# Performance work log

Measured on AMD Instinct MI355X. Metric: run time of the kernel, lower is better.

## Reference

```python
import jax, jax.numpy as jnp
import numpy as np

K = 3       # kernel_size
RATE = 2    # dilation rate
NH = 8      # num_heads
EPS = 1e-5  # InstanceNorm eps


def _conv1x1(x, W, b):
    # x: [B,C,H,W], W: [O,C], b: [O]
    return jnp.einsum('bchw,oc->bohw', x, W) + b[None, :, None, None]


def _inorm(x):
    mu = jnp.mean(x, axis=(2, 3), keepdims=True)
    var = jnp.var(x, axis=(2, 3), keepdims=True)
    return (x - mu) / jnp.sqrt(var + EPS)


def _extract_patches(x):
    # dilated KxK patches, stride 1, 'same' grid -> [B, C, K*K, H, W]
    B, C, H, W = x.shape
    pad = RATE * (K - 1) // 2
    xp = jnp.pad(x, ((0, 0), (0, 0), (pad, pad), (pad, pad)))
    taps = [xp[:, :, i * RATE:i * RATE + H, j * RATE:j * RATE + W]
            for i in range(K) for j in range(K)]
    return jnp.stack(taps, axis=2)


def setup_inputs() -> dict:
    key = jax.random.key(0)
    ks = jax.random.split(key, 8)
    B, C, H, W, A = 1, 64, 64, 64, 128
    features = jax.random.normal(ks[0], (B, C, H, W), jnp.float32)
    masks = jax.random.uniform(ks[1], (B, 1, H, W), jnp.float32)
    s_in = 1.0 / np.sqrt(C).astype(np.float32)
    Wq = jax.random.normal(ks[2], (A, C), jnp.float32) * s_in
    bq = jnp.zeros((A,), jnp.float32)
    Wk = jax.random.normal(ks[3], (A, C), jnp.float32) * s_in
    bk = jnp.zeros((A,), jnp.float32)
    Wo = jax.random.normal(ks[4], (C, C), jnp.float32) * s_in
    bo = jnp.zeros((C,), jnp.float32)
    return dict(features=features, masks=masks, Wq=Wq, bq=bq,
                Wk=Wk, bk=bk, Wo=Wo, bo=bo)


def reference(features, masks, Wq, bq, Wk, bk, Wo, bo):
    B, C, H, W = features.shape
    A = Wq.shape[0]
    hc = A // NH
    L = H * W
    KK = K * K

    m = (masks > 0.5).astype(features.dtype)          # 1 = hole
    f_masked = features * m
    f_unmasked = features * (1.0 - m)

    q = jax.nn.relu(_inorm(_conv1x1(f_masked, Wq, bq)))    # [B,A,H,W]
    k = jax.nn.relu(_inorm(_conv1x1(f_unmasked, Wk, bk)))  # [B,A,H,W]

    # per-head dilated patch banks: [B,NH,hc*KK,L]
    qp = _extract_patches(q).reshape(B, NH, hc * KK, L)
    kp = _extract_patches(k).reshape(B, NH, hc * KK, L)

    # patch-correlation attention per head: [B,NH,L,L]
    attn = jax.nn.softmax(jnp.einsum('bndq,bndk->bnqk', qp, kp), axis=-1)

    # value patch bank from unmasked features: [B,C*KK,L]
    vp = _extract_patches(f_unmasked).reshape(B, C * KK, L)

    # sample value patches: [B,NH,L,C*KK]
    sampled = jnp.einsum('bnqk,bdk->bnqd', attn, vp)

    # fold: average the KK taps per channel, then average over heads
    attended = sampled.reshape(B, NH, L, C, KK).mean(axis=4).mean(axis=1)  # [B,L,C]
    attended = attended.transpose(0, 2, 1).reshape(B, C, H, W)

    return jax.nn.relu(_inorm(_conv1x1(attended, Wo, bo)))
```

## Files before the change

### kernel.cpp

```cpp
#include <hip/hip_runtime.h>
#include <hip/hip_bf16.h>


#define LL 4096
#define CC 64
#define AA 128
#define NH_ 8
#define KSTR 168
#define VSTR 72
#define LOG2E 1.44269504088896340736f

typedef _Float16 half8 __attribute__((ext_vector_type(8)));
typedef float floatx4 __attribute__((ext_vector_type(4)));

__device__ __forceinline__ float fexp2(float x) {
    float r;
    asm("v_exp_f32 %0, %1" : "=v"(r) : "v"(x));
    return r;
}

__global__ __launch_bounds__(256) void prep_kernel(
    const float* __restrict__ feat,
    const float* __restrict__ masks,
    const float* __restrict__ Wq, const float* __restrict__ bq,
    const float* __restrict__ Wk, const float* __restrict__ bk,
    _Float16* __restrict__ q_act, _Float16* __restrict__ k_act,
    _Float16* __restrict__ vb)
{
    const int tid = threadIdx.x;
    const int b = blockIdx.x;
    __shared__ float sW[CC];
    __shared__ float sm[8];

    if (b >= 2 * AA) {
        int c = b - 2 * AA;
        for (int p = 0; p < 16; ++p) {
            int l = p * 256 + tid;
            int y = l >> 6, x = l & 63;
            float s = 0.f;
            for (int ty = 0; ty < 3; ++ty) {
                int yy = y + 2 * (ty - 1);
                if (yy < 0 || yy > 63) continue;
                for (int tx = 0; tx < 3; ++tx) {
                    int xx = x + 2 * (tx - 1);
                    if (xx < 0 || xx > 63) continue;
                    int ll = yy * 64 + xx;
                    float hole = masks[ll] > 0.5f ? 1.f : 0.f;
                    s += feat[c * LL + ll] * (1.f - hole);
                }
            }
            vb[c * LL + l] = (_Float16)(s * (1.f / 9.f));
        }
        return;
    }

    const int a = b & (AA - 1);
    const int sel = b >> 7;
    const float* Wrow = (sel ? Wk : Wq) + a * CC;
    const float bias = sel ? bk[a] : bq[a];
    if (tid < CC) sW[tid] = Wrow[tid];
    __syncthreads();

    float acc[16];
#pragma unroll
    for (int p = 0; p < 16; ++p) acc[p] = 0.f;
    for (int c = 0; c < CC; ++c) {
        float wc = sW[c];
        const float* fr = feat + (size_t)c * LL + tid;
#pragma unroll
        for (int p = 0; p < 16; ++p) acc[p] += wc * fr[p * 256];
    }

    float vals[16];
    float s1 = 0.f, s2 = 0.f;
#pragma unroll
    for (int p = 0; p < 16; ++p) {
        int l = p * 256 + tid;
        float hole = masks[l] > 0.5f ? 1.f : 0.f;
        float mf = sel ? (1.f - hole) : hole;
        float v = acc[p] * mf + bias;
        vals[p] = v; s1 += v; s2 += v * v;
    }
    for (int off = 32; off; off >>= 1) {
        s1 += __shfl_down(s1, off, 64);
        s2 += __shfl_down(s2, off, 64);
    }
    int wv = tid >> 6, ln = tid & 63;
    if (ln == 0) { sm[wv * 2] = s1; sm[wv * 2 + 1] = s2; }
    __syncthreads();
    s1 = sm[0] + sm[2] + sm[4] + sm[6];
    s2 = sm[1] + sm[3] + sm[5] + sm[7];
    float mu = s1 * (1.f / LL);
    float inv = rsqrtf(s2 * (1.f / LL) - mu * mu + 1e-5f);

    const float oscale = sel ? 1.f : LOG2E;
    _Float16* act = (sel ? k_act : q_act) + (size_t)a * LL;
#pragma unroll
    for (int p = 0; p < 16; ++p) {
        int l = p * 256 + tid;
        float v = (vals[p] - mu) * inv;
        act[l] = (_Float16)(v > 0.f ? v * oscale : 0.f);
    }
}

__global__ __launch_bounds__(256) void build_kp(
    const _Float16* __restrict__ k_act, _Float16* __restrict__ kp)
{
    const int n = blockIdx.x, y = blockIdx.y;
    const int tid = threadIdx.x;
    const _Float16* ka = k_act + (size_t)n * 16 * LL;
    _Float16* base = kp + ((size_t)n * LL + y * 64) * KSTR;
#pragma unroll
    for (int i = 0; i < 6; ++i) {
        int idx = tid + i * 256;
        if (idx >= 64 * 21) break;
        int x = idx / 21, c21 = idx - x * 21;
        half8 v8;
#pragma unroll
        for (int j = 0; j < 8; ++j) {
            int d = c21 * 8 + j;
            _Float16 v = (_Float16)0.f;
            if (d < 144) {
                int ah = d / 9, t = d - ah * 9;
                int ty = t / 3, tx = t - ty * 3;
                int yy = y + 2 * (ty - 1);
                int xx = x + 2 * (tx - 1);
                if (yy >= 0 && yy <= 63 && xx >= 0 && xx <= 63)
                    v = ka[ah * LL + yy * 64 + xx];
            }
            v8[j] = v;
        }
        *(half8*)(base + (size_t)idx * 8) = v8;
    }
}

__global__ __launch_bounds__(512, 4) void attn_kernel(
    const _Float16* __restrict__ q_act, const _Float16* __restrict__ kp,
    const _Float16* __restrict__ vb,
    _Float16* __restrict__ Opart, float* __restrict__ ml)
{
    const int qt2 = blockIdx.x, n = blockIdx.y, h = blockIdx.z;
    const int jt0 = h * 32;
    const int tid = threadIdx.x;
    const int w = tid >> 6, lane = tid & 63;
    const int wq = w >> 2, wx = w & 3;
    const int y = qt2 * 2 + wq;
    const int l15 = lane & 15, quad = lane >> 4;

    __shared__ __align__(16) _Float16 Bk[2][64 * KSTR];
    __shared__ __align__(16) _Float16 Vt[2][64 * VSTR];
    __shared__ __align__(16) _Float16 Pb[8][16 * VSTR];

    const _Float16* kpn = kp + (size_t)n * LL * KSTR;
    const uint4* vbu = (const uint4*)vb;

    const int vc = tid >> 3, ve = tid & 7;

    auto issue_bk = [&](int jt, _Float16* dst) {
        const char* tile = (const char*)(kpn + (size_t)jt * 64 * KSTR) + (lane << 4);
        for (int c = w; c < 21; c += 8) {
            __builtin_amdgcn_global_load_lds(
                (const __attribute__((address_space(1))) void*)(tile + c * 1024),
                (__attribute__((address_space(3))) void*)(dst + c * 512),
                16, 0, 0);
        }
    };

    half8 afrag[5];
    {
        const _Float16* qa = q_act + (size_t)n * 16 * LL;
        const int x = wx * 16 + l15;
#pragma unroll
        for (int ks = 0; ks < 5; ++ks) {
#pragma unroll
            for (int j = 0; j < 8; ++j) {
                int d = ks * 32 + quad * 8 + j;
                _Float16 v = (_Float16)0.f;
                if (d < 144) {
                    int ah = d / 9, t = d - ah * 9;
                    int ty = t / 3, tx = t - ty * 3;
                    int yy = y + 2 * (ty - 1);
                    int xx = x + 2 * (tx - 1);
                    if (yy >= 0 && yy <= 63 && xx >= 0 && xx <= 63)
                        v = qa[ah * LL + yy * 64 + xx];
                }
                afrag[ks][j] = v;
            }
        }
    }

    floatx4 accO[4];
    float mrow[4], lrow[4];
#pragma unroll
    for (int i = 0; i < 4; ++i) {
        accO[i] = (floatx4){0.f, 0.f, 0.f, 0.f};
        mrow[i] = -1e30f; lrow[i] = 0.f;
    }

    uint4 vreg;
    issue_bk(jt0, Bk[0]);
    vreg = vbu[vc * (LL / 8) + jt0 * 8 + ve];

    int cur = 0;
    for (int it = 0; it < 32; ++it) {
        ((uint4*)Vt[cur])[vc * 9 + ve] = vreg;

        __syncthreads();

        if (it < 31) {
            const int jn = jt0 + it + 1;
            issue_bk(jn, Bk[cur ^ 1]);
            vreg = vbu[vc * (LL / 8) + jn * 8 + ve];
        }

        const _Float16* bk = Bk[cur];
        const _Float16* vt = Vt[cur];

        floatx4 accS[4];
#pragma unroll
        for (int i = 0; i < 4; ++i) accS[i] = (floatx4){0.f, 0.f, 0.f, 0.f};
        __builtin_amdgcn_s_setprio(1);
        for (int ks = 0; ks < 5; ++ks) {
#pragma unroll
            for (int nt = 0; nt < 4; ++nt) {
                half8 bfr = *(const half8*)(bk + (nt * 16 + l15) * KSTR + ks * 32 + quad * 8);
                accS[nt] = __builtin_amdgcn_mfma_f32_16x16x32_f16(afrag[ks], bfr, accS[nt], 0, 0, 0);
            }
        }
        __builtin_amdgcn_s_setprio(0);

#pragma unroll
        for (int r = 0; r < 4; ++r) {
            float tm = fmaxf(fmaxf(accS[0][r], accS[1][r]), fmaxf(accS[2][r], accS[3][r]));
            if (!__all(tm <= mrow[r] + 3.0f)) {
#pragma unroll
                for (int off = 8; off; off >>= 1) tm = fmaxf(tm, __shfl_xor(tm, off, 16));
                float mn = fmaxf(mrow[r], tm);
                float alpha = fexp2(mrow[r] - mn);
                mrow[r] = mn;
                lrow[r] *= alpha;
#pragma unroll
                for (int nt = 0; nt < 4; ++nt) accO[nt][r] *= alpha;
            }
            float rs = 0.f;
#pragma unroll
            for (int nt = 0; nt < 4; ++nt) {
                float pv = fexp2(accS[nt][r] - mrow[r]);
                accS[nt][r] = pv;
                rs += pv;
            }
            lrow[r] += rs;
        }

        _Float16* pw = Pb[w];
#pragma unroll
        for (int nt = 0; nt < 4; ++nt)
#pragma unroll
            for (int r = 0; r < 4; ++r)
                pw[(quad * 4 + r) * VSTR + ((nt ^ quad) << 4) + l15] = (_Float16)accS[nt][r];

        __builtin_amdgcn_s_setprio(1);
#pragma unroll
        for (int ks = 0; ks < 2; ++ks) {
            int kb = ks * 2 + (quad >> 1);
            half8 afr = *(const half8*)(pw + l15 * VSTR + ((kb ^ (l15 >> 2)) << 4) + (quad & 1) * 8);
#pragma unroll
            for (int nt = 0; nt < 4; ++nt) {
                half8 bfr = *(const half8*)(vt + (nt * 16 + l15) * VSTR + ks * 32 + quad * 8);
                accO[nt] = __builtin_amdgcn_mfma_f32_16x16x32_f16(afr, bfr, accO[nt], 0, 0, 0);
            }
        }
        __builtin_amdgcn_s_setprio(0);

        cur ^= 1;
    }

#pragma unroll
    for (int r = 0; r < 4; ++r) {
        float rs = lrow[r];
#pragma unroll
        for (int off = 8; off; off >>= 1) rs += __shfl_xor(rs, off, 16);
        lrow[r] = rs;
    }

    _Float16* op = Opart + ((size_t)(n * 2 + h) * LL + y * 64 + wx * 16) * CC;
#pragma unroll
    for (int r = 0; r < 4; ++r) {
        float invl = 1.f / lrow[r];
        int row = quad * 4 + r;
#pragma unroll
        for (int nt = 0; nt < 4; ++nt)
            op[row * CC + nt * 16 + l15] = (_Float16)(accO[nt][r] * invl);
        if (l15 == 0) {
            float* mlp = ml + ((size_t)n * LL + y * 64 + wx * 16 + row) * 4;
            mlp[2 * h] = mrow[r];
            mlp[2 * h + 1] = lrow[r];
        }
    }
}

__global__ __launch_bounds__(256) void combine_kernel(
    const _Float16* __restrict__ Opart, const float* __restrict__ ml,
    float* __restrict__ att)
{
    int t = blockIdx.x * 256 + threadIdx.x;
    int l = t >> 6, c = t & 63;
    float s = 0.f;
#pragma unroll
    for (int n = 0; n < NH_; ++n) {
        const float* mlp = ml + ((size_t)n * LL + l) * 4;
        float m0 = mlp[0], l0 = mlp[1], m1 = mlp[2], l1 = mlp[3];
        float M = fmaxf(m0, m1);
        float w0 = l0 * fexp2(m0 - M);
        float w1 = l1 * fexp2(m1 - M);
        float o0 = (float)Opart[((size_t)(2 * n) * LL + l) * CC + c];
        float o1 = (float)Opart[((size_t)(2 * n + 1) * LL + l) * CC + c];
        s += (w0 * o0 + w1 * o1) / (w0 + w1);
    }
    att[t] = s * 0.125f;
}

__global__ __launch_bounds__(256) void out_kernel(
    const float* __restrict__ att,
    const float* __restrict__ Wo, const float* __restrict__ bo,
    float* __restrict__ out)
{
    const int o = blockIdx.x;
    const int tid = threadIdx.x;
    __shared__ float sW[CC];
    __shared__ float sm[8];
    if (tid < CC) sW[tid] = Wo[o * CC + tid];
    __syncthreads();
    const float bias = bo[o];

    float vals[16], s1 = 0.f, s2 = 0.f;
    for (int p = 0; p < 16; ++p) {
        int l = p * 256 + tid;
        const float4* arow = (const float4*)(att + (size_t)l * CC);
        float acc = bias;
#pragma unroll
        for (int c4 = 0; c4 < 16; ++c4) {
            float4 a4 = arow[c4];
            acc += sW[c4 * 4] * a4.x + sW[c4 * 4 + 1] * a4.y +
                   sW[c4 * 4 + 2] * a4.z + sW[c4 * 4 + 3] * a4.w;
        }
        vals[p] = acc; s1 += acc; s2 += acc * acc;
    }
    for (int off = 32; off; off >>= 1) {
        s1 += __shfl_down(s1, off, 64);
        s2 += __shfl_down(s2, off, 64);
    }
    int wv = tid >> 6, ln = tid & 63;
    if (ln == 0) { sm[wv * 2] = s1; sm[wv * 2 + 1] = s2; }
    __syncthreads();
    s1 = sm[0] + sm[2] + sm[4] + sm[6];
    s2 = sm[1] + sm[3] + sm[5] + sm[7];
    float mu = s1 * (1.f / LL);
    float inv = rsqrtf(s2 * (1.f / LL) - mu * mu + 1e-5f);
    for (int p = 0; p < 16; ++p) {
        int l = p * 256 + tid;
        float v = (vals[p] - mu) * inv;
        out[(size_t)o * LL + l] = v > 0.f ? v : 0.f;
    }
}

extern "C" void kernel_launch(void* const* d_in, const int* in_sizes, int n_in,
                              void* d_out, int out_size, void* d_ws, size_t ws_size,
                              hipStream_t stream) {
    const float* feat  = (const float*)d_in[0];
    const float* masks = (const float*)d_in[1];
    const float* Wq    = (const float*)d_in[2];
    const float* bq    = (const float*)d_in[3];
    const float* Wk    = (const float*)d_in[4];
    const float* bk    = (const float*)d_in[5];
    const float* Wo    = (const float*)d_in[6];
    const float* bo    = (const float*)d_in[7];
    float* out = (float*)d_out;

    char* ws = (char*)d_ws;
    _Float16* q_act = (_Float16*)ws;
    _Float16* k_act = (_Float16*)(ws + 1048576);
    _Float16* vb    = (_Float16*)(ws + 2097152);
    float*    att   = (float*)(ws + 2621440);
    _Float16* kp    = (_Float16*)(ws + 3670016);
    _Float16* Opart = (_Float16*)(ws + 14680064);
    float*    ml    = (float*)(ws + 23068672);

    prep_kernel<<<2 * AA + CC, 256, 0, stream>>>(feat, masks, Wq, bq, Wk, bk,
                                                 q_act, k_act, vb);
    dim3 gb(NH_, 64);
    build_kp<<<gb, 256, 0, stream>>>(k_act, kp);
    dim3 g(32, NH_, 2);
    attn_kernel<<<g, 512, 0, stream>>>(q_act, kp, vb, Opart, ml);
    combine_kernel<<<LL * CC / 256, 256, 0, stream>>>(Opart, ml, att);
    out_kernel<<<CC, 256, 0, stream>>>(att, Wo, bo, out);
}
```

Baseline: 242.5 us.

## Have each attention wave process two query rows to reuse K/V fragments

Result: no change. 245.8 us (+1.4%).

```diff
diff --git a/kernel.cpp b/kernel.cpp
--- a/kernel.cpp
+++ b/kernel.cpp
@@ -134,7 +134,7 @@
     }
 }
 
-__global__ __launch_bounds__(512, 4) void attn_kernel(
+__global__ __launch_bounds__(256, 2) void attn_kernel(
     const _Float16* __restrict__ q_act, const _Float16* __restrict__ kp,
     const _Float16* __restrict__ vb,
     _Float16* __restrict__ Opart, float* __restrict__ ml)
@@ -143,22 +143,21 @@
     const int jt0 = h * 32;
     const int tid = threadIdx.x;
     const int w = tid >> 6, lane = tid & 63;
-    const int wq = w >> 2, wx = w & 3;
-    const int y = qt2 * 2 + wq;
     const int l15 = lane & 15, quad = lane >> 4;
 
     __shared__ __align__(16) _Float16 Bk[2][64 * KSTR];
     __shared__ __align__(16) _Float16 Vt[2][64 * VSTR];
-    __shared__ __align__(16) _Float16 Pb[8][16 * VSTR];
+    __shared__ __align__(16) _Float16 Pb[4][2][16 * VSTR];
 
     const _Float16* kpn = kp + (size_t)n * LL * KSTR;
     const uint4* vbu = (const uint4*)vb;
 
-    const int vc = tid >> 3, ve = tid & 7;
+    const int vc0 = tid >> 3, ve0 = tid & 7;
+    const int vc1 = (tid + 256) >> 3, ve1 = tid & 7;
 
     auto issue_bk = [&](int jt, _Float16* dst) {
         const char* tile = (const char*)(kpn + (size_t)jt * 64 * KSTR) + (lane << 4);
-        for (int c = w; c < 21; c += 8) {
+        for (int c = w; c < 21; c += 4) {
             __builtin_amdgcn_global_load_lds(
                 (const __attribute__((address_space(1))) void*)(tile + c * 1024),
                 (__attribute__((address_space(3))) void*)(dst + c * 512),
@@ -166,108 +165,130 @@
         }
     };
 
-    half8 afrag[5];
+    half8 afrag[2][5];
     {
         const _Float16* qa = q_act + (size_t)n * 16 * LL;
-        const int x = wx * 16 + l15;
-#pragma unroll
-        for (int ks = 0; ks < 5; ++ks) {
-#pragma unroll
-            for (int j = 0; j < 8; ++j) {
-                int d = ks * 32 + quad * 8 + j;
-                _Float16 v = (_Float16)0.f;
-                if (d < 144) {
-                    int ah = d / 9, t = d - ah * 9;
-                    int ty = t / 3, tx = t - ty * 3;
-                    int yy = y + 2 * (ty - 1);
-                    int xx = x + 2 * (tx - 1);
-                    if (yy >= 0 && yy <= 63 && xx >= 0 && xx <= 63)
-                        v = qa[ah * LL + yy * 64 + xx];
+        const int x = w * 16 + l15;
+#pragma unroll
+        for (int rs = 0; rs < 2; ++rs) {
+            const int y = qt2 * 2 + rs;
+#pragma unroll
+            for (int ks = 0; ks < 5; ++ks) {
+#pragma unroll
+                for (int j = 0; j < 8; ++j) {
+                    int d = ks * 32 + quad * 8 + j;
+                    _Float16 v = (_Float16)0.f;
+                    if (d < 144) {
+                        int ah = d / 9, t = d - ah * 9;
+                        int ty = t / 3, tx = t - ty * 3;
+                        int yy = y + 2 * (ty - 1);
+                        int xx = x + 2 * (tx - 1);
+                        if (yy >= 0 && yy <= 63 && xx >= 0 && xx <= 63)
+                            v = qa[ah * LL + yy * 64 + xx];
+                    }
+                    afrag[rs][ks][j] = v;
                 }
-                afrag[ks][j] = v;
-            }
-        }
-    }
-
-    floatx4 accO[4];
-    float mrow[4], lrow[4];
-#pragma unroll
-    for (int i = 0; i < 4; ++i) {
-        accO[i] = (floatx4){0.f, 0.f, 0.f, 0.f};
-        mrow[i] = -1e30f; lrow[i] = 0.f;
-    }
-
-    uint4 vreg;
+            }
+        }
+    }
+
+    floatx4 accO[2][4];
+    float mrow[2][4], lrow[2][4];
+#pragma unroll
+    for (int rs = 0; rs < 2; ++rs)
+#pragma unroll
+        for (int i = 0; i < 4; ++i) {
+            accO[rs][i] = (floatx4){0.f, 0.f, 0.f, 0.f};
+            mrow[rs][i] = -1e30f; lrow[rs][i] = 0.f;
+        }
+
+    uint4 vreg[2];
     issue_bk(jt0, Bk[0]);
-    vreg = vbu[vc * (LL / 8) + jt0 * 8 + ve];
+    vreg[0] = vbu[vc0 * (LL / 8) + jt0 * 8 + ve0];
+    vreg[1] = vbu[vc1 * (LL / 8) + jt0 * 8 + ve1];
 
     int cur = 0;
     for (int it = 0; it < 32; ++it) {
-        ((uint4*)Vt[cur])[vc * 9 + ve] = vreg;
+        {
+            uint4* vd = (uint4*)Vt[cur];
+            vd[vc0 * 9 + ve0] = vreg[0];
+            vd[vc1 * 9 + ve1] = vreg[1];
+        }
 
         __syncthreads();
 
         if (it < 31) {
             const int jn = jt0 + it + 1;
             issue_bk(jn, Bk[cur ^ 1]);
-            vreg = vbu[vc * (LL / 8) + jn * 8 + ve];
+            vreg[0] = vbu[vc0 * (LL / 8) + jn * 8 + ve0];
+            vreg[1] = vbu[vc1 * (LL / 8) + jn * 8 + ve1];
         }
 
         const _Float16* bk = Bk[cur];
         const _Float16* vt = Vt[cur];
 
-        floatx4 accS[4];
-#pragma unroll
-        for (int i = 0; i < 4; ++i) accS[i] = (floatx4){0.f, 0.f, 0.f, 0.f};
+        floatx4 accS[2][4];
+#pragma unroll
+        for (int rs = 0; rs < 2; ++rs)
+#pragma unroll
+            for (int i = 0; i < 4; ++i) accS[rs][i] = (floatx4){0.f, 0.f, 0.f, 0.f};
         __builtin_amdgcn_s_setprio(1);
         for (int ks = 0; ks < 5; ++ks) {
 #pragma unroll
             for (int nt = 0; nt < 4; ++nt) {
                 half8 bfr = *(const half8*)(bk + (nt * 16 + l15) * KSTR + ks * 32 + quad * 8);
-                accS[nt] = __builtin_amdgcn_mfma_f32_16x16x32_f16(afrag[ks], bfr, accS[nt], 0, 0, 0);
+                accS[0][nt] = __builtin_amdgcn_mfma_f32_16x16x32_f16(afrag[0][ks], bfr, accS[0][nt], 0, 0, 0);
+                accS[1][nt] = __builtin_amdgcn_mfma_f32_16x16x32_f16(afrag[1][ks], bfr, accS[1][nt], 0, 0, 0);
             }
         }
         __builtin_amdgcn_s_setprio(0);
 
 #pragma unroll
-        for (int r = 0; r < 4; ++r) {
-            float tm = fmaxf(fmaxf(accS[0][r], accS[1][r]), fmaxf(accS[2][r], accS[3][r]));
-            if (!__all(tm <= mrow[r] + 3.0f)) {
-#pragma unroll
-                for (int off = 8; off; off >>= 1) tm = fmaxf(tm, __shfl_xor(tm, off, 16));
-                float mn = fmaxf(mrow[r], tm);
-                float alpha = fexp2(mrow[r] - mn);
-                mrow[r] = mn;
-                lrow[r] *= alpha;
-#pragma unroll
-                for (int nt = 0; nt < 4; ++nt) accO[nt][r] *= alpha;
-            }
-            float rs = 0.f;
-#pragma unroll
-            for (int nt = 0; nt < 4; ++nt) {
-                float pv = fexp2(accS[nt][r] - mrow[r]);
-                accS[nt][r] = pv;
-                rs += pv;
-            }
-            lrow[r] += rs;
-        }
-
-        _Float16* pw = Pb[w];
-#pragma unroll
-        for (int nt = 0; nt < 4; ++nt)
-#pragma unroll
-            for (int r = 0; r < 4; ++r)
-                pw[(quad * 4 + r) * VSTR + ((nt ^ quad) << 4) + l15] = (_Float16)accS[nt][r];
+        for (int rs = 0; rs < 2; ++rs) {
+#pragma unroll
+            for (int r = 0; r < 4; ++r) {
+                float tm = fmaxf(fmaxf(accS[rs][0][r], accS[rs][1][r]),
+                                 fmaxf(accS[rs][2][r], accS[rs][3][r]));
+                if (!__all(tm <= mrow[rs][r] + 3.0f)) {
+#pragma unroll
+                    for (int off = 8; off; off >>= 1) tm = fmaxf(tm, __shfl_xor(tm, off, 16));
+                    float mn = fmaxf(mrow[rs][r], tm);
+                    float alpha = fexp2(mrow[rs][r] - mn);
+                    mrow[rs][r] = mn;
+                    lrow[rs][r] *= alpha;
+#pragma unroll
+                    for (int nt = 0; nt < 4; ++nt) accO[rs][nt][r] *= alpha;
+                }
+                float rsum = 0.f;
+#pragma unroll
+                for (int nt = 0; nt < 4; ++nt) {
+                    float pv = fexp2(accS[rs][nt][r] - mrow[rs][r]);
+                    accS[rs][nt][r] = pv;
+                    rsum += pv;
+                }
+                lrow[rs][r] += rsum;
+            }
+
+            _Float16* pw = Pb[w][rs];
+#pragma unroll
+            for (int nt = 0; nt < 4; ++nt)
+#pragma unroll
+                for (int r = 0; r < 4; ++r)
+                    pw[(quad * 4 + r) * VSTR + ((nt ^ quad) << 4) + l15] = (_Float16)accS[rs][nt][r];
+        }
 
         __builtin_amdgcn_s_setprio(1);
 #pragma unroll
         for (int ks = 0; ks < 2; ++ks) {
             int kb = ks * 2 + (quad >> 1);
-            half8 afr = *(const half8*)(pw + l15 * VSTR + ((kb ^ (l15 >> 2)) << 4) + (quad & 1) * 8);
+            const int poff = l15 * VSTR + ((kb ^ (l15 >> 2)) << 4) + (quad & 1) * 8;
+            half8 afr0 = *(const half8*)(Pb[w][0] + poff);
+            half8 afr1 = *(const half8*)(Pb[w][1] + poff);
 #pragma unroll
             for (int nt = 0; nt < 4; ++nt) {
                 half8 bfr = *(const half8*)(vt + (nt * 16 + l15) * VSTR + ks * 32 + quad * 8);
-                accO[nt] = __builtin_amdgcn_mfma_f32_16x16x32_f16(afr, bfr, accO[nt], 0, 0, 0);
+                accO[0][nt] = __builtin_amdgcn_mfma_f32_16x16x32_f16(afr0, bfr, accO[0][nt], 0, 0, 0);
+                accO[1][nt] = __builtin_amdgcn_mfma_f32_16x16x32_f16(afr1, bfr, accO[1][nt], 0, 0, 0);
             }
         }
         __builtin_amdgcn_s_setprio(0);
@@ -276,25 +297,29 @@
     }
 
 #pragma unroll
-    for (int r = 0; r < 4; ++r) {
-        float rs = lrow[r];
-#pragma unroll
-        for (int off = 8; off; off >>= 1) rs += __shfl_xor(rs, off, 16);
-        lrow[r] = rs;
-    }
-
-    _Float16* op = Opart + ((size_t)(n * 2 + h) * LL + y * 64 + wx * 16) * CC;
-#pragma unroll
-    for (int r = 0; r < 4; ++r) {
-        float invl = 1.f / lrow[r];
-        int row = quad * 4 + r;
-#pragma unroll
-        for (int nt = 0; nt < 4; ++nt)
-            op[row * CC + nt * 16 + l15] = (_Float16)(accO[nt][r] * invl);
-        if (l15 == 0) {
-            float* mlp = ml + ((size_t)n * LL + y * 64 + wx * 16 + row) * 4;
-            mlp[2 * h] = mrow[r];
-            mlp[2 * h + 1] = lrow[r];
+    for (int rs = 0; rs < 2; ++rs) {
+        const int y = qt2 * 2 + rs;
+#pragma unroll
+        for (int r = 0; r < 4; ++r) {
+            float rsum = lrow[rs][r];
+#pragma unroll
+            for (int off = 8; off; off >>= 1) rsum += __shfl_xor(rsum, off, 16);
+            lrow[rs][r] = rsum;
+        }
+
+        _Float16* op = Opart + ((size_t)(n * 2 + h) * LL + y * 64 + w * 16) * CC;
+#pragma unroll
+        for (int r = 0; r < 4; ++r) {
+            float invl = 1.f / lrow[rs][r];
+            int row = quad * 4 + r;
+#pragma unroll
+            for (int nt = 0; nt < 4; ++nt)
+                op[row * CC + nt * 16 + l15] = (_Float16)(accO[rs][nt][r] * invl);
+            if (l15 == 0) {
+                float* mlp = ml + ((size_t)n * LL + y * 64 + w * 16 + row) * 4;
+                mlp[2 * h] = mrow[rs][r];
+                mlp[2 * h + 1] = lrow[rs][r];
+            }
         }
     }
 }
@@ -391,7 +416,7 @@
     dim3 gb(NH_, 64);
     build_kp<<<gb, 256, 0, stream>>>(k_act, kp);
     dim3 g(32, NH_, 2);
-    attn_kernel<<<g, 512, 0, stream>>>(q_act, kp, vb, Opart, ml);
+    attn_kernel<<<g, 256, 0, stream>>>(q_act, kp, vb, Opart, ml);
     combine_kernel<<<LL * CC / 256, 256, 0, stream>>>(Opart, ml, att);
     out_kernel<<<CC, 256, 0, stream>>>(att, Wo, bo, out);
 }
```
